# Kernel optimization log

Hardware: AMD Instinct MI355X
Metric: run time of the kernel (lower is better)

Reference implementation:

```python
import jax, jax.numpy as jnp
import numpy as np

UNITS = 256
BATCH = 256


def _make_sizes():
    rng = np.random.default_rng(0)
    nclasses = rng.integers(2, 16, size=BATCH).astype(np.int32)
    nfeature = rng.integers(50, 201, size=BATCH).astype(np.int32)
    return nclasses, nfeature


def setup_inputs() -> dict:
    key = jax.random.key(0)
    nclasses, nfeature = _make_sizes()
    total = int((nclasses.astype(np.int64) * nfeature).sum())
    x = jax.random.normal(key, (total, UNITS), dtype=jnp.float32)
    return {
        "x": x,
        "nclasses": jnp.asarray(nclasses),
        "nfeature": jnp.asarray(nfeature),
    }


def reference(x, nclasses, nfeature):
    # sizes[i] = nclasses[i] * nfeature[i]; segment i covers rows [start_i, start_i + sizes_i)
    sizes = (nclasses * nfeature).astype(jnp.int32)          # [B]
    num_segments = sizes.shape[0]
    ends = jnp.cumsum(sizes)                                  # [B]
    # segment id of each row: first segment whose end exceeds the row index
    seg_ids = jnp.searchsorted(ends, jnp.arange(x.shape[0]), side="right")
    sums = jax.ops.segment_sum(x, seg_ids, num_segments=num_segments)  # [B, units]
    return sums / sizes[:, None].astype(x.dtype)              # per-segment mean
```

## Files before the change

### kernel.cpp

```cpp
#include <hip/hip_runtime.h>

#define UNITS 256
#define BATCH 256

typedef float fx4 __attribute__((ext_vector_type(4)));

__global__ __launch_bounds__(256) void k_zero(float* __restrict__ out) {
    const int i = (blockIdx.x * 256 + threadIdx.x) << 2;
    *reinterpret_cast<fx4*>(out + i) = fx4{0.f, 0.f, 0.f, 0.f};
}

__global__ __launch_bounds__(256) void k_accum(const float* __restrict__ x,
                                               const int* __restrict__ nclasses,
                                               const int* __restrict__ nfeature,
                                               float* __restrict__ out,
                                               int total_rows, int lo, int nE4) {
    __shared__ int   s_ends[BATCH];
    __shared__ float s_inv[BATCH];
    __shared__ int   s_wsum[4];
    __shared__ float s_red[4][64][4];
    const int t  = threadIdx.x;
    const int ln = t & 63;
    const int rl = t >> 6;

    {
        const int sz = nclasses[t] * nfeature[t];
        s_inv[t] = 1.0f / (float)sz;
        int v = sz;
        #pragma unroll
        for (int off = 1; off < 64; off <<= 1) {
            int u = __shfl_up(v, off, 64);
            if (ln >= off) v += u;
        }
        if (ln == 63) s_wsum[rl] = v;
        __syncthreads();
        int base = 0;
        #pragma unroll
        for (int w = 0; w < 3; ++w)
            if (w < rl) base += s_wsum[w];
        s_ends[t] = v + base;
        __syncthreads();
    }

    const int b    = blockIdx.x;
    const int hi   = lo + 4;
    const int r0   = (b < nE4) ? b * hi : nE4 * hi + (b - nE4) * lo;
    const int csz  = (b < nE4) ? hi : lo;
    const int rend = min(r0 + csz, total_rows);
    if (r0 >= rend) return;

    int slo = 0, shi = BATCH;
    while (slo < shi) {
        int mid = (slo + shi) >> 1;
        if (s_ends[mid] > r0) shi = mid; else slo = mid + 1;
    }
    int seg = slo;

    const int c = ln << 2;
    int r = r0 + rl;
    const float* p = x + (size_t)r * UNITS + c;
    fx4 acc = {0.f, 0.f, 0.f, 0.f};

    for (;;) {
        const int stop = min(s_ends[seg], rend);
        int cnt = (stop - r + 3) >> 2;
        if (cnt < 0) cnt = 0;
        r += cnt << 2;

        int k = 0;
        for (; k + 4 <= cnt; k += 4) {
            fx4 v0 = *(const fx4*)(p);
            fx4 v1 = *(const fx4*)(p + 4  * UNITS);
            fx4 v2 = *(const fx4*)(p + 8  * UNITS);
            fx4 v3 = *(const fx4*)(p + 12 * UNITS);
            p += 16 * UNITS;
            acc += (v0 + v1) + (v2 + v3);
        }
        for (; k < cnt; ++k) {
            fx4 v = *(const fx4*)(p);
            p += 4 * UNITS;
            acc += v;
        }

        *reinterpret_cast<fx4*>(&s_red[rl][ln][0]) = acc;
        __syncthreads();
        {
            const int q  = t >> 2, e = t & 3;
            const float vsum = s_red[0][q][e] + s_red[1][q][e]
                             + s_red[2][q][e] + s_red[3][q][e];
            unsafeAtomicAdd(out + seg * UNITS + t, vsum * s_inv[seg]);
        }
        if (s_ends[seg] >= rend) break;
        ++seg;
        acc = fx4{0.f, 0.f, 0.f, 0.f};
        __syncthreads();
    }
}

extern "C" void kernel_launch(void* const* d_in, const int* in_sizes, int n_in,
                              void* d_out, int out_size, void* d_ws, size_t ws_size,
                              hipStream_t stream) {
    const float* x        = (const float*)d_in[0];
    const int*   nclasses = (const int*)d_in[1];
    const int*   nfeature = (const int*)d_in[2];
    float*       out      = (float*)d_out;

    const int total_rows = in_sizes[0] / UNITS;

    const int q   = total_rows >> 11;
    const int lo  = q & ~3;
    const int E   = total_rows - (lo << 11);
    const int nE4 = (E + 3) >> 2;

    k_zero<<<64, 256, 0, stream>>>(out);
    k_accum<<<2048, 256, 0, stream>>>(x, nclasses, nfeature, out,
                                      total_rows, lo, nE4);
}
```

Measured before the change: 53.91 us.

## Give each wave a contiguous row slice and merge segment partials once

Measured after the change: 55.02 us. +2.1%, slower.

```diff
diff --git a/kernel.cpp b/kernel.cpp
--- a/kernel.cpp
+++ b/kernel.cpp
@@ -10,15 +10,16 @@
     *reinterpret_cast<fx4*>(out + i) = fx4{0.f, 0.f, 0.f, 0.f};
 }
 
-__global__ __launch_bounds__(256) void k_accum(const float* __restrict__ x,
-                                               const int* __restrict__ nclasses,
-                                               const int* __restrict__ nfeature,
-                                               float* __restrict__ out,
-                                               int total_rows, int lo, int nE4) {
+__global__ __launch_bounds__(256, 8) void k_accum(const float* __restrict__ x,
+                                                  const int* __restrict__ nclasses,
+                                                  const int* __restrict__ nfeature,
+                                                  float* __restrict__ out,
+                                                  int total_rows, int lo, int nE4) {
     __shared__ int   s_ends[BATCH];
     __shared__ float s_inv[BATCH];
     __shared__ int   s_wsum[4];
-    __shared__ float s_red[4][64][4];
+    __shared__ int   s_seg[4][2];
+    __shared__ float s_red[4][2][256];
     const int t  = threadIdx.x;
     const int ln = t & 63;
     const int rl = t >> 6;
@@ -49,51 +50,72 @@
     const int rend = min(r0 + csz, total_rows);
     if (r0 >= rend) return;
 
+    const int wq = csz >> 2;
+    const int ws = min(r0 + rl * wq, rend);
+    const int we = min(r0 + (rl + 1) * wq, rend);
+
+    const int key = min(ws, rend - 1);
     int slo = 0, shi = BATCH;
     while (slo < shi) {
         int mid = (slo + shi) >> 1;
-        if (s_ends[mid] > r0) shi = mid; else slo = mid + 1;
+        if (s_ends[mid] > key) shi = mid; else slo = mid + 1;
     }
     int seg = slo;
 
-    const int c = ln << 2;
-    int r = r0 + rl;
-    const float* p = x + (size_t)r * UNITS + c;
+    const float* p = x + (size_t)ws * UNITS + (ln << 2);
+    int r = ws;
     fx4 acc = {0.f, 0.f, 0.f, 0.f};
 
-    for (;;) {
-        const int stop = min(s_ends[seg], rend);
-        int cnt = (stop - r + 3) >> 2;
+    #pragma unroll
+    for (int run = 0; run < 2; ++run) {
+        const int stop = min(s_ends[seg], we);
+        int cnt = stop - r;
         if (cnt < 0) cnt = 0;
-        r += cnt << 2;
+        r += cnt;
 
         int k = 0;
         for (; k + 4 <= cnt; k += 4) {
             fx4 v0 = *(const fx4*)(p);
-            fx4 v1 = *(const fx4*)(p + 4  * UNITS);
-            fx4 v2 = *(const fx4*)(p + 8  * UNITS);
-            fx4 v3 = *(const fx4*)(p + 12 * UNITS);
-            p += 16 * UNITS;
+            fx4 v1 = *(const fx4*)(p + UNITS);
+            fx4 v2 = *(const fx4*)(p + 2 * UNITS);
+            fx4 v3 = *(const fx4*)(p + 3 * UNITS);
+            p += 4 * UNITS;
             acc += (v0 + v1) + (v2 + v3);
         }
         for (; k < cnt; ++k) {
             fx4 v = *(const fx4*)(p);
-            p += 4 * UNITS;
+            p += UNITS;
             acc += v;
         }
 
-        *reinterpret_cast<fx4*>(&s_red[rl][ln][0]) = acc;
-        __syncthreads();
-        {
-            const int q  = t >> 2, e = t & 3;
-            const float vsum = s_red[0][q][e] + s_red[1][q][e]
-                             + s_red[2][q][e] + s_red[3][q][e];
-            unsafeAtomicAdd(out + seg * UNITS + t, vsum * s_inv[seg]);
+        if (ln == 0) s_seg[rl][run] = seg;
+        *reinterpret_cast<fx4*>(&s_red[rl][run][ln << 2]) = acc;
+        acc = fx4{0.f, 0.f, 0.f, 0.f};
+        if (r < we) ++seg;
+    }
+    __syncthreads();
+
+    {
+        const int seg0 = s_seg[0][0];
+        float a0 = 0.f, a1 = 0.f, a2 = 0.f;
+        int maxd = 0;
+        #pragma unroll
+        for (int w = 0; w < 4; ++w) {
+            #pragma unroll
+            for (int run = 0; run < 2; ++run) {
+                const int d = s_seg[w][run] - seg0;
+                const float v = s_red[w][run][t];
+                a0 += (d == 0) ? v : 0.f;
+                a1 += (d == 1) ? v : 0.f;
+                a2 += (d == 2) ? v : 0.f;
+                maxd = max(maxd, d);
+            }
         }
-        if (s_ends[seg] >= rend) break;
-        ++seg;
-        acc = fx4{0.f, 0.f, 0.f, 0.f};
-        __syncthreads();
+        unsafeAtomicAdd(out + seg0 * UNITS + t, a0 * s_inv[seg0]);
+        if (maxd >= 1)
+            unsafeAtomicAdd(out + (seg0 + 1) * UNITS + t, a1 * s_inv[seg0 + 1]);
+        if (maxd >= 2)
+            unsafeAtomicAdd(out + (seg0 + 2) * UNITS + t, a2 * s_inv[seg0 + 2]);
     }
 }
 
```

## Replace atomic segment accumulation with per-block partials and a deterministic final reduction

Applied to the files above, without the earlier changes.

New measurement: 59.00 us. 1.09x slower.

```diff
diff --git a/kernel.cpp b/kernel.cpp
--- a/kernel.cpp
+++ b/kernel.cpp
@@ -2,71 +2,74 @@
 
 #define UNITS 256
 #define BATCH 256
+#define NBLK  2048
 
 typedef float fx4 __attribute__((ext_vector_type(4)));
 
-__global__ __launch_bounds__(256) void k_zero(float* __restrict__ out) {
-    const int i = (blockIdx.x * 256 + threadIdx.x) << 2;
-    *reinterpret_cast<fx4*>(out + i) = fx4{0.f, 0.f, 0.f, 0.f};
+__device__ __forceinline__ void scan_sizes(const int* __restrict__ nclasses,
+                                           const int* __restrict__ nfeature,
+                                           int* s_ends, int* s_wsum,
+                                           int t, int ln, int rl) {
+    int v = nclasses[t] * nfeature[t];
+    #pragma unroll
+    for (int off = 1; off < 64; off <<= 1) {
+        int u = __shfl_up(v, off, 64);
+        if (ln >= off) v += u;
+    }
+    if (ln == 63) s_wsum[rl] = v;
+    __syncthreads();
+    int base = 0;
+    #pragma unroll
+    for (int w = 0; w < 3; ++w)
+        if (w < rl) base += s_wsum[w];
+    s_ends[t] = v + base;
+    __syncthreads();
 }
 
-__global__ __launch_bounds__(256) void k_accum(const float* __restrict__ x,
-                                               const int* __restrict__ nclasses,
-                                               const int* __restrict__ nfeature,
-                                               float* __restrict__ out,
-                                               int total_rows, int lo, int nE4) {
+__global__ __launch_bounds__(256, 8) void k_part(const float* __restrict__ x,
+                                                 const int* __restrict__ nclasses,
+                                                 const int* __restrict__ nfeature,
+                                                 float* __restrict__ part,
+                                                 int* __restrict__ pseg,
+                                                 int total_rows, int lo, int nE4) {
     __shared__ int   s_ends[BATCH];
-    __shared__ float s_inv[BATCH];
     __shared__ int   s_wsum[4];
-    __shared__ float s_red[4][64][4];
-    const int t  = threadIdx.x;
-    const int ln = t & 63;
-    const int rl = t >> 6;
-
-    {
-        const int sz = nclasses[t] * nfeature[t];
-        s_inv[t] = 1.0f / (float)sz;
-        int v = sz;
-        #pragma unroll
-        for (int off = 1; off < 64; off <<= 1) {
-            int u = __shfl_up(v, off, 64);
-            if (ln >= off) v += u;
-        }
-        if (ln == 63) s_wsum[rl] = v;
-        __syncthreads();
-        int base = 0;
-        #pragma unroll
-        for (int w = 0; w < 3; ++w)
-            if (w < rl) base += s_wsum[w];
-        s_ends[t] = v + base;
-        __syncthreads();
-    }
+    __shared__ int   s_seg[4][3];
+    __shared__ float s_red[4][3][256];
+    const int t = threadIdx.x, ln = t & 63, rl = t >> 6;
+    scan_sizes(nclasses, nfeature, s_ends, s_wsum, t, ln, rl);
 
     const int b    = blockIdx.x;
     const int hi   = lo + 4;
     const int r0   = (b < nE4) ? b * hi : nE4 * hi + (b - nE4) * lo;
     const int csz  = (b < nE4) ? hi : lo;
     const int rend = min(r0 + csz, total_rows);
-    if (r0 >= rend) return;
+    if (r0 >= rend) {
+        #pragma unroll
+        for (int d = 0; d < 3; ++d) part[(b * 3 + d) * 256 + t] = 0.f;
+        if (t == 0) pseg[b] = 0;
+        return;
+    }
 
-    int slo = 0, shi = BATCH;
-    while (slo < shi) {
-        int mid = (slo + shi) >> 1;
-        if (s_ends[mid] > r0) shi = mid; else slo = mid + 1;
+    int r = r0 + rl;
+    const int key = min(r, rend - 1);
+    int bl = 0, bh = BATCH;
+    while (bl < bh) {
+        int mid = (bl + bh) >> 1;
+        if (s_ends[mid] > key) bh = mid; else bl = mid + 1;
     }
-    int seg = slo;
+    int seg = bl;
 
-    const int c = ln << 2;
-    int r = r0 + rl;
-    const float* p = x + (size_t)r * UNITS + c;
-    fx4 acc = {0.f, 0.f, 0.f, 0.f};
+    const float* p = x + (size_t)r * UNITS + (ln << 2);
 
-    for (;;) {
+    #pragma unroll
+    for (int run = 0; run < 3; ++run) {
         const int stop = min(s_ends[seg], rend);
         int cnt = (stop - r + 3) >> 2;
         if (cnt < 0) cnt = 0;
         r += cnt << 2;
 
+        fx4 acc = {0.f, 0.f, 0.f, 0.f};
         int k = 0;
         for (; k + 4 <= cnt; k += 4) {
             fx4 v0 = *(const fx4*)(p);
@@ -82,19 +85,62 @@
             acc += v;
         }
 
-        *reinterpret_cast<fx4*>(&s_red[rl][ln][0]) = acc;
-        __syncthreads();
-        {
-            const int q  = t >> 2, e = t & 3;
-            const float vsum = s_red[0][q][e] + s_red[1][q][e]
-                             + s_red[2][q][e] + s_red[3][q][e];
-            unsafeAtomicAdd(out + seg * UNITS + t, vsum * s_inv[seg]);
+        if (ln == 0) s_seg[rl][run] = seg;
+        *reinterpret_cast<fx4*>(&s_red[rl][run][ln << 2]) = acc;
+        if (s_ends[seg] <= r && r < rend) ++seg;
+    }
+    __syncthreads();
+
+    const int seg0 = s_seg[0][0];
+    float a0 = 0.f, a1 = 0.f, a2 = 0.f;
+    #pragma unroll
+    for (int w = 0; w < 4; ++w) {
+        #pragma unroll
+        for (int run = 0; run < 3; ++run) {
+            const int d = s_seg[w][run] - seg0;
+            const float v = s_red[w][run][t];
+            a0 += (d == 0) ? v : 0.f;
+            a1 += (d == 1) ? v : 0.f;
+            a2 += (d == 2) ? v : 0.f;
         }
-        if (s_ends[seg] >= rend) break;
-        ++seg;
-        acc = fx4{0.f, 0.f, 0.f, 0.f};
-        __syncthreads();
     }
+    part[(b * 3 + 0) * 256 + t] = a0;
+    part[(b * 3 + 1) * 256 + t] = a1;
+    part[(b * 3 + 2) * 256 + t] = a2;
+    if (t == 0) pseg[b] = seg0;
+}
+
+__global__ __launch_bounds__(256, 8) void k_final(const float* __restrict__ part,
+                                                  const int* __restrict__ pseg,
+                                                  const int* __restrict__ nclasses,
+                                                  const int* __restrict__ nfeature,
+                                                  float* __restrict__ out,
+                                                  int total_rows, int lo, int nE4) {
+    __shared__ int s_ends[BATCH];
+    __shared__ int s_wsum[4];
+    const int t = threadIdx.x, ln = t & 63, rl = t >> 6;
+    scan_sizes(nclasses, nfeature, s_ends, s_wsum, t, ln, rl);
+
+    const int i     = blockIdx.x;
+    const int start = (i == 0) ? 0 : s_ends[i - 1];
+    const int end   = s_ends[i];
+    const int hi    = lo + 4;
+    const int tierA = nE4 * hi;
+
+    const int Rl = start, Rr = end - 1;
+    int b_first = (Rl < tierA) ? (Rl / hi)
+                               : (lo ? nE4 + (Rl - tierA) / lo : NBLK - 1);
+    int b_last  = (Rr < tierA) ? (Rr / hi)
+                               : (lo ? nE4 + (Rr - tierA) / lo : NBLK - 1);
+    if (b_last >= NBLK) b_last = NBLK - 1;
+
+    float sum = 0.f;
+    for (int b = b_first; b <= b_last; ++b) {
+        const int d = i - pseg[b];
+        if (0 <= d && d <= 2) sum += part[(b * 3 + d) * 256 + t];
+    }
+    const float inv = 1.0f / (float)(nclasses[i] * nfeature[i]);
+    out[i * UNITS + t] = sum * inv;
 }
 
 extern "C" void kernel_launch(void* const* d_in, const int* in_sizes, int n_in,
@@ -104,6 +150,8 @@
     const int*   nclasses = (const int*)d_in[1];
     const int*   nfeature = (const int*)d_in[2];
     float*       out      = (float*)d_out;
+    float*       part     = (float*)d_ws;
+    int*         pseg     = (int*)((char*)d_ws + NBLK * 3 * 256 * sizeof(float));
 
     const int total_rows = in_sizes[0] / UNITS;
 
@@ -112,7 +160,8 @@
     const int E   = total_rows - (lo << 11);
     const int nE4 = (E + 3) >> 2;
 
-    k_zero<<<64, 256, 0, stream>>>(out);
-    k_accum<<<2048, 256, 0, stream>>>(x, nclasses, nfeature, out,
-                                      total_rows, lo, nE4);
+    k_part<<<NBLK, 256, 0, stream>>>(x, nclasses, nfeature, part, pseg,
+                                     total_rows, lo, nE4);
+    k_final<<<BATCH, 256, 0, stream>>>(part, pseg, nclasses, nfeature, out,
+                                       total_rows, lo, nE4);
 }
```
